# Optimization experiments

Hardware: AMD Instinct MI355X
Metric: run time of the kernel (lower is better)

## Reference

```python
import jax, jax.numpy as jnp
import numpy as np

DELTA = 0.1
T_FEATS = 16384  # static: ds.sum() = 2*1024*8, durations are fixed at 8 in setup_inputs


def setup_inputs() -> dict:
    key = jax.random.key(0)
    k1, _ = jax.random.split(key)
    hs = jax.random.normal(k1, (2, 1024, 512), dtype=jnp.float32)  # (B, T_text, adim)
    ds = jnp.full((2, 1024), 8, dtype=jnp.int32)                   # (B, T_text) token durations
    return {"hs": hs, "ds": ds}


def reference(hs, ds):
    # Gaussian upsampling (https://arxiv.org/abs/2010.04301), fixed temperature.
    ds_f = ds.astype(jnp.float32)
    # token centers: cumsum(d) - d/2, shape (B, T_text)
    c = jnp.cumsum(ds_f, axis=-1) - ds_f / 2.0
    # output frame positions, shape (T_feats,)
    t = jnp.arange(T_FEATS, dtype=jnp.float32)
    # energy (B, T_feats, T_text): -delta * (t - c)^2
    energy = -DELTA * (t[None, :, None] - c[:, None, :]) ** 2
    p_attn = jax.nn.softmax(energy, axis=2)
    # weighted sum of hidden states: (B, T_feats, adim)
    return jnp.einsum("bft,btd->bfd", p_attn, hs)
```

## Files before the change

kernel.cpp:

```cpp
#include <hip/hip_runtime.h>
#include <math.h>


#define T_TEXT   1024
#define ADIM     512
#define TFEATS   16384
#define DELTA_F  0.1f
#define FR       32
#define W        4
#define KW       (2*W + 1)
#define STAGE    16

__global__ __launch_bounds__(1024) void centers_kernel(const int* __restrict__ ds,
                                                       float* __restrict__ c) {
    const int b = blockIdx.x;
    const int j = threadIdx.x;
    __shared__ float buf[T_TEXT];
    const float d = (float)ds[b * T_TEXT + j];
    float x = d;
    buf[j] = x;
    __syncthreads();
    for (int off = 1; off < T_TEXT; off <<= 1) {
        float y = 0.f;
        if (j >= off) y = buf[j - off];
        __syncthreads();
        if (j >= off) { x += y; buf[j] = x; }
        __syncthreads();
    }
    c[b * T_TEXT + j] = x - 0.5f * d;
}

__global__ __launch_bounds__(256) void upsample_kernel(const float* __restrict__ hs,
                                                       const float* __restrict__ c,
                                                       float* __restrict__ out) {
    __shared__ float s_hs[STAGE * ADIM];
    __shared__ float s_w[FR][KW];
    __shared__ int   s_jb[FR];

    const int tile = blockIdx.x;
    const int b    = blockIdx.y;
    const int f0   = tile * FR;
    const int tid  = threadIdx.x;

    const float* __restrict__ cb = c + b * T_TEXT;

    if (tid < FR) {
        const float t = (float)(f0 + tid);
        int lo = 0, hi = T_TEXT;
        while (lo < hi) {
            const int mid = (lo + hi) >> 1;
            if (cb[mid] < t) lo = mid + 1; else hi = mid;
        }
        int j0 = (lo >= T_TEXT) ? (T_TEXT - 1) : lo;
        if (j0 > 0 && (t - cb[j0 - 1] <= cb[j0] - t)) --j0;
        int jb = j0 - W;
        if (jb < 0) jb = 0;
        if (jb > T_TEXT - KW) jb = T_TEXT - KW;
        s_jb[tid] = jb;

        float e[KW];
        float m = -INFINITY;
        #pragma unroll
        for (int k = 0; k < KW; ++k) {
            const float dd = t - cb[jb + k];
            e[k] = -DELTA_F * dd * dd;
            m = fmaxf(m, e[k]);
        }
        float s = 0.f;
        #pragma unroll
        for (int k = 0; k < KW; ++k) { e[k] = __expf(e[k] - m); s += e[k]; }
        const float inv = 1.f / s;
        #pragma unroll
        for (int k = 0; k < KW; ++k) s_w[tid][k] = e[k] * inv;
    }
    __syncthreads();

    const int jlo = s_jb[0];
    int span = s_jb[FR - 1] + KW - jlo;
    if (span > STAGE) span = STAGE;

    const float* __restrict__ hsb = hs + (size_t)b * T_TEXT * ADIM;
    const int d2 = 2 * tid;
    for (int r = 0; r < span; ++r) {
        *(float2*)(&s_hs[r * ADIM + d2]) =
            *(const float2*)(&hsb[(size_t)(jlo + r) * ADIM + d2]);
    }
    __syncthreads();

    float* __restrict__ outb = out + ((size_t)b * TFEATS + f0) * ADIM + d2;
    for (int f = 0; f < FR; ++f) {
        int off = s_jb[f] - jlo;
        if (off > STAGE - KW) off = STAGE - KW;
        const float* hrow = &s_hs[off * ADIM + d2];
        float ax = 0.f, ay = 0.f;
        #pragma unroll
        for (int k = 0; k < KW; ++k) {
            const float w = s_w[f][k];
            const float2 h = *(const float2*)(&hrow[k * ADIM]);
            ax = fmaf(w, h.x, ax);
            ay = fmaf(w, h.y, ay);
        }
        *(float2*)(&outb[(size_t)f * ADIM]) = make_float2(ax, ay);
    }
}

extern "C" void kernel_launch(void* const* d_in, const int* in_sizes, int n_in,
                              void* d_out, int out_size, void* d_ws, size_t ws_size,
                              hipStream_t stream) {
    const float* hs = (const float*)d_in[0];
    const int*   ds = (const int*)d_in[1];
    float* out = (float*)d_out;
    float* c   = (float*)d_ws;

    const int B = in_sizes[1] / T_TEXT;

    centers_kernel<<<dim3(B), dim3(T_TEXT), 0, stream>>>(ds, c);
    upsample_kernel<<<dim3(TFEATS / FR, B), dim3(256), 0, stream>>>(hs, c, out);
}
```

Measured before the change: 90.74 us.

## Fuse center cumsum into upsample kernel and group frames sharing a window

Drops the separate centers kernel. Each upsample block now recomputes the token-center prefix sum in shared memory with a wavefront shuffle scan, which removes one launch and the global round trip for the centers. The inner loop switches to float4 loads and stores and lets consecutive frames with the same window start share each loaded hidden row. The cost is redundant per-block scan work over 1024 durations and data-dependent branching over group sizes.

```diff
diff --git a/kernel.cpp b/kernel.cpp
--- a/kernel.cpp
+++ b/kernel.cpp
@@ -2,57 +2,91 @@
 #include <math.h>
 
 
-#define T_TEXT   1024
-#define ADIM     512
-#define TFEATS   16384
-#define DELTA_F  0.1f
-#define FR       32
-#define W        4
-#define KW       (2*W + 1)
-#define STAGE    16
+#define T_TEXT  1024
+#define ADIM    512
+#define TFEATS  16384
+#define DELTA_F 0.1f
+#define FR      32
+#define W       4
+#define KW      (2*W + 1)
+#define STAGE   16
+#define WPAD    12
 
-__global__ __launch_bounds__(1024) void centers_kernel(const int* __restrict__ ds,
-                                                       float* __restrict__ c) {
-    const int b = blockIdx.x;
-    const int j = threadIdx.x;
-    __shared__ float buf[T_TEXT];
-    const float d = (float)ds[b * T_TEXT + j];
-    float x = d;
-    buf[j] = x;
-    __syncthreads();
-    for (int off = 1; off < T_TEXT; off <<= 1) {
-        float y = 0.f;
-        if (j >= off) y = buf[j - off];
-        __syncthreads();
-        if (j >= off) { x += y; buf[j] = x; }
-        __syncthreads();
+template <int L>
+__device__ __forceinline__ void group_fma(const float* __restrict__ hp,
+                                          const float (*__restrict__ sw)[WPAD],
+                                          int f, float* __restrict__ op) {
+    float w[L][KW];
+    #pragma unroll
+    for (int l = 0; l < L; ++l) {
+        const float4 wa = *(const float4*)&sw[f + l][0];
+        const float4 wb = *(const float4*)&sw[f + l][4];
+        w[l][0] = wa.x; w[l][1] = wa.y; w[l][2] = wa.z; w[l][3] = wa.w;
+        w[l][4] = wb.x; w[l][5] = wb.y; w[l][6] = wb.z; w[l][7] = wb.w;
+        w[l][8] = sw[f + l][8];
     }
-    c[b * T_TEXT + j] = x - 0.5f * d;
+    float4 acc[L];
+    #pragma unroll
+    for (int l = 0; l < L; ++l) acc[l] = make_float4(0.f, 0.f, 0.f, 0.f);
+    #pragma unroll
+    for (int k = 0; k < KW; ++k) {
+        const float4 h = *(const float4*)&hp[k * ADIM];
+        #pragma unroll
+        for (int l = 0; l < L; ++l) {
+            acc[l].x = fmaf(w[l][k], h.x, acc[l].x);
+            acc[l].y = fmaf(w[l][k], h.y, acc[l].y);
+            acc[l].z = fmaf(w[l][k], h.z, acc[l].z);
+            acc[l].w = fmaf(w[l][k], h.w, acc[l].w);
+        }
+    }
+    #pragma unroll
+    for (int l = 0; l < L; ++l) *(float4*)&op[(size_t)l * ADIM] = acc[l];
 }
 
-__global__ __launch_bounds__(256) void upsample_kernel(const float* __restrict__ hs,
-                                                       const float* __restrict__ c,
-                                                       float* __restrict__ out) {
+__global__ __launch_bounds__(256) void gup_kernel(const float* __restrict__ hs,
+                                                  const int* __restrict__ ds,
+                                                  float* __restrict__ out) {
     __shared__ float s_hs[STAGE * ADIM];
-    __shared__ float s_w[FR][KW];
+    __shared__ float s_c[T_TEXT];
+    __shared__ float s_w[FR][WPAD];
     __shared__ int   s_jb[FR];
+    __shared__ int   s_wt[4];
 
-    const int tile = blockIdx.x;
-    const int b    = blockIdx.y;
-    const int f0   = tile * FR;
-    const int tid  = threadIdx.x;
+    const int tid = threadIdx.x;
+    const int b   = blockIdx.y;
+    const int f0  = blockIdx.x * FR;
 
-    const float* __restrict__ cb = c + b * T_TEXT;
+    const int4 dv = *(const int4*)(ds + b * T_TEXT + 4 * tid);
+    const int p0 = dv.x, p1 = p0 + dv.y, p2 = p1 + dv.z, p3 = p2 + dv.w;
+    int x = p3;
+    const int lane = tid & 63;
+    #pragma unroll
+    for (int off = 1; off < 64; off <<= 1) {
+        const int y = __shfl_up(x, off, 64);
+        if (lane >= off) x += y;
+    }
+    const int wid = tid >> 6;
+    if (lane == 63) s_wt[wid] = x;
+    __syncthreads();
+    int woff = 0;
+    #pragma unroll
+    for (int w2 = 0; w2 < 4; ++w2) if (w2 < wid) woff += s_wt[w2];
+    const int ebase = woff + x - p3;
+    s_c[4 * tid + 0] = (float)(ebase + p0) - 0.5f * (float)dv.x;
+    s_c[4 * tid + 1] = (float)(ebase + p1) - 0.5f * (float)dv.y;
+    s_c[4 * tid + 2] = (float)(ebase + p2) - 0.5f * (float)dv.z;
+    s_c[4 * tid + 3] = (float)(ebase + p3) - 0.5f * (float)dv.w;
+    __syncthreads();
 
     if (tid < FR) {
         const float t = (float)(f0 + tid);
         int lo = 0, hi = T_TEXT;
         while (lo < hi) {
             const int mid = (lo + hi) >> 1;
-            if (cb[mid] < t) lo = mid + 1; else hi = mid;
+            if (s_c[mid] < t) lo = mid + 1; else hi = mid;
         }
         int j0 = (lo >= T_TEXT) ? (T_TEXT - 1) : lo;
-        if (j0 > 0 && (t - cb[j0 - 1] <= cb[j0] - t)) --j0;
+        if (j0 > 0 && (t - s_c[j0 - 1] <= s_c[j0] - t)) --j0;
         int jb = j0 - W;
         if (jb < 0) jb = 0;
         if (jb > T_TEXT - KW) jb = T_TEXT - KW;
@@ -62,7 +96,7 @@
         float m = -INFINITY;
         #pragma unroll
         for (int k = 0; k < KW; ++k) {
-            const float dd = t - cb[jb + k];
+            const float dd = t - s_c[jb + k];
             e[k] = -DELTA_F * dd * dd;
             m = fmaxf(m, e[k]);
         }
@@ -78,29 +112,35 @@
     const int jlo = s_jb[0];
     int span = s_jb[FR - 1] + KW - jlo;
     if (span > STAGE) span = STAGE;
-
-    const float* __restrict__ hsb = hs + (size_t)b * T_TEXT * ADIM;
-    const int d2 = 2 * tid;
-    for (int r = 0; r < span; ++r) {
-        *(float2*)(&s_hs[r * ADIM + d2]) =
-            *(const float2*)(&hsb[(size_t)(jlo + r) * ADIM + d2]);
+    const float* __restrict__ hsb = hs + ((size_t)b * T_TEXT + jlo) * ADIM;
+    const int total4 = span * (ADIM / 4);
+    for (int i = tid; i < total4; i += 256) {
+        *(float4*)&s_hs[4 * i] = *(const float4*)&hsb[4 * i];
     }
     __syncthreads();
 
-    float* __restrict__ outb = out + ((size_t)b * TFEATS + f0) * ADIM + d2;
-    for (int f = 0; f < FR; ++f) {
-        int off = s_jb[f] - jlo;
+    const int d4    = 4 * (tid & 127);
+    const int fbase = (tid >> 7) * 16;
+    float* __restrict__ outB = out + ((size_t)b * TFEATS + f0 + fbase) * ADIM + d4;
+
+    int i = 0;
+    while (i < 16) {
+        const int f  = fbase + i;
+        const int jb = s_jb[f];
+        int L = 1;
+        while (L < 4 && i + L < 16 && s_jb[f + L] == jb) ++L;
+        int off = jb - jlo;
+        if (off < 0) off = 0;
         if (off > STAGE - KW) off = STAGE - KW;
-        const float* hrow = &s_hs[off * ADIM + d2];
-        float ax = 0.f, ay = 0.f;
-        #pragma unroll
-        for (int k = 0; k < KW; ++k) {
-            const float w = s_w[f][k];
-            const float2 h = *(const float2*)(&hrow[k * ADIM]);
-            ax = fmaf(w, h.x, ax);
-            ay = fmaf(w, h.y, ay);
+        const float* hp = &s_hs[off * ADIM + d4];
+        float* op = outB + (size_t)i * ADIM;
+        switch (L) {
+            case 4: group_fma<4>(hp, s_w, f, op); break;
+            case 3: group_fma<3>(hp, s_w, f, op); break;
+            case 2: group_fma<2>(hp, s_w, f, op); break;
+            default: group_fma<1>(hp, s_w, f, op); break;
         }
-        *(float2*)(&outb[(size_t)f * ADIM]) = make_float2(ax, ay);
+        i += L;
     }
 }
 
@@ -110,10 +150,7 @@
     const float* hs = (const float*)d_in[0];
     const int*   ds = (const int*)d_in[1];
     float* out = (float*)d_out;
-    float* c   = (float*)d_ws;
-
     const int B = in_sizes[1] / T_TEXT;
 
-    centers_kernel<<<dim3(B), dim3(T_TEXT), 0, stream>>>(ds, c);
-    upsample_kernel<<<dim3(TFEATS / FR, B), dim3(256), 0, stream>>>(hs, c, out);
+    gup_kernel<<<dim3(TFEATS / FR, B), dim3(256), 0, stream>>>(hs, ds, out);
 }
```

Result: faster. 85.51 us (-5.8%).
